# Kernel tuning notes

Hardware: AMD Instinct MI355X
Metric: run time of the kernel (lower is better)

## Reference

```python
import jax, jax.numpy as jnp
import numpy as np

TOPK = 13
ALPHA = 1.0
BETA = 6.0
EPS = 1e-9


def _make_boxes(key, shape, img=640.0, min_sz=10.0, max_sz=110.0):
    k1, k2 = jax.random.split(key)
    cxcy = jax.random.uniform(k1, shape[:-1] + (2,)) * img
    wh = min_sz + jax.random.uniform(k2, shape[:-1] + (2,)) * (max_sz - min_sz)
    return jnp.concatenate([cxcy - wh / 2, cxcy + wh / 2], axis=-1)


def setup_inputs() -> dict:
    key = jax.random.key(0)
    ks = jax.random.split(key, 8)
    B, L, C, n, K = 16, 8400, 1, 32, 68
    pred_scores = jax.random.uniform(ks[0], (B, L, C))
    pred_bboxes = _make_boxes(ks[1], (B, L, 4))
    anchor_points = jax.random.uniform(ks[2], (L, 2)) * 640.0
    gt_labels = jax.random.randint(ks[3], (B, n, 1), 0, C).astype(jnp.int64)
    gt_bboxes = _make_boxes(ks[4], (B, n, 4))
    gt_poses = jax.random.normal(ks[5], (B, n, K, 3))
    gt_vertices = jax.random.normal(ks[6], (B, n, K, 3))
    gt_rotations = jax.random.normal(ks[7], (B, n, 3, 3))
    pad_gt_mask = jnp.ones((B, n, 1), jnp.float32)
    return {"pred_scores": pred_scores, "pred_bboxes": pred_bboxes,
            "anchor_points": anchor_points, "gt_labels": gt_labels,
            "gt_bboxes": gt_bboxes, "gt_poses": gt_poses,
            "gt_vertices": gt_vertices, "gt_rotations": gt_rotations,
            "pad_gt_mask": pad_gt_mask, "bg_index": 1}


def batch_iou_similarity(box1, box2):
    # box1 [B,n,4], box2 [B,L,4] -> [B,n,L]
    b1 = box1[:, :, None, :]
    b2 = box2[:, None, :, :]
    x1y1 = jnp.maximum(b1[..., :2], b2[..., :2])
    x2y2 = jnp.minimum(b1[..., 2:], b2[..., 2:])
    overlap = jnp.clip(x2y2 - x1y1, 0).prod(-1)
    area1 = jnp.clip(b1[..., 2:] - b1[..., :2], 0).prod(-1)
    area2 = jnp.clip(b2[..., 2:] - b2[..., :2], 0).prod(-1)
    return overlap / (area1 + area2 - overlap + EPS)


def check_points_inside_bboxes(points, bboxes):
    # points [L,2], bboxes [B,n,4] -> [B,n,L] float
    x = points[None, None, :, 0]
    y = points[None, None, :, 1]
    xmin, ymin, xmax, ymax = jnp.split(bboxes[:, :, None, :], 4, axis=-1)
    deltas = jnp.stack([x - xmin[..., 0], y - ymin[..., 0],
                        xmax[..., 0] - x, ymax[..., 0] - y], axis=-1)
    return (deltas.min(-1) > EPS).astype(bboxes.dtype)


def gather_topk_anchors(metrics, topk, topk_mask):
    # metrics [B,n,L], topk_mask [B,n,1] -> [B,n,L]
    L = metrics.shape[-1]
    _, topk_idxs = jax.lax.top_k(metrics, topk)  # [B,n,topk]
    is_in_topk = jax.nn.one_hot(topk_idxs, L, dtype=metrics.dtype).sum(-2)
    return is_in_topk * topk_mask


def compute_max_iou_anchor(ious):
    # [B,n,L] -> one-hot over gt dim of per-anchor argmax iou
    n = ious.shape[1]
    idx = ious.argmax(axis=1)  # [B,L]
    return jnp.transpose(jax.nn.one_hot(idx, n, dtype=ious.dtype), (0, 2, 1))


def reference(pred_scores, pred_bboxes, anchor_points, gt_labels, gt_bboxes,
              gt_poses, gt_vertices, gt_rotations, pad_gt_mask, bg_index):
    B, L, C = pred_scores.shape
    n = gt_bboxes.shape[1]
    K = gt_poses.shape[2]

    ious = batch_iou_similarity(gt_bboxes, pred_bboxes)  # [B,n,L]
    ps_t = jnp.transpose(pred_scores, (0, 2, 1))  # [B,C,L]
    lbl = gt_labels[..., 0]  # [B,n]
    bbox_cls_scores = jnp.take_along_axis(ps_t, lbl[:, :, None], axis=1)  # [B,n,L]

    alignment_metrics = (bbox_cls_scores ** ALPHA) * (ious ** BETA)
    is_in_gts = check_points_inside_bboxes(anchor_points, gt_bboxes)
    is_in_topk = gather_topk_anchors(alignment_metrics * is_in_gts, TOPK, pad_gt_mask)
    mask_positive = is_in_topk * is_in_gts * pad_gt_mask  # [B,n,L]
    mask_positive_sum = mask_positive.sum(axis=1)  # [B,L]

    # resolve anchors assigned to multiple gts by max IoU (no-op when none)
    mask_multiple = jnp.broadcast_to((mask_positive_sum[:, None, :] > 1), mask_positive.shape)
    is_max_iou = compute_max_iou_anchor(ious)
    mask_positive = jnp.where(mask_multiple, is_max_iou, mask_positive)
    mask_positive_sum = mask_positive.sum(axis=1)

    batch_ind = jnp.arange(B, dtype=jnp.int32)[:, None]
    assigned_gt_index = mask_positive.argmax(axis=1)  # [B,L]
    assigned_gt_index = assigned_gt_index + batch_ind * n
    flat_idx = assigned_gt_index.reshape(-1)

    assigned_labels = gt_labels.reshape(-1)[flat_idx].reshape(B, L)
    assigned_labels = jnp.where(mask_positive_sum > 0, assigned_labels, bg_index)

    assigned_bboxes = gt_bboxes.reshape(-1, 4)[flat_idx].reshape(B, L, 4)
    assigned_poses = gt_poses.reshape(-1, K, 3)[flat_idx].reshape(B, L, K, 3)
    assigned_vertices = gt_vertices.reshape(-1, K, 3)[flat_idx].reshape(B, L, K, 3)
    assigned_rotations = gt_rotations.reshape(-1, 3, 3)[flat_idx].reshape(B, L, 3, 3)

    scores_oh = jax.nn.one_hot(assigned_labels, C + 1, dtype=pred_scores.dtype)
    keep = jnp.array([i for i in range(C + 1) if i != bg_index], dtype=jnp.int32)
    assigned_scores = scores_oh[..., keep]  # [B,L,C]

    am = alignment_metrics * mask_positive
    max_metrics_per_instance = am.max(axis=-1, keepdims=True)
    max_ious_per_instance = (ious * mask_positive).max(axis=-1, keepdims=True)
    am = am / (max_metrics_per_instance + EPS) * max_ious_per_instance
    am = am.max(axis=1)[:, :, None]  # [B,L,1]
    assigned_scores = assigned_scores * am

    return (assigned_labels, assigned_bboxes, assigned_scores, assigned_poses,
            assigned_vertices, assigned_rotations, assigned_gt_index)
```

## Files before the change

kernel.cpp:

```cpp
#include <hip/hip_runtime.h>

#define Bn 16
#define Ln 8400
#define Cn 1
#define Ngt 32
#define Kpt 68
#define TOPKN 13
#define EPSF 1e-9f
#define CAP 2048

typedef unsigned int u32;

#define OFF_LABELS   0
#define OFF_BBOXES   134400
#define OFF_SCORES   672000
#define OFF_POSES    806400
#define OFF_VERTS    28224000
#define OFF_ROT      55641600
#define OFF_GTIDX    56851200

__device__ __forceinline__ float iou_box(float gx0, float gy0, float gx1, float gy1,
                                         float4 p) {
    float ix0 = fmaxf(gx0, p.x), iy0 = fmaxf(gy0, p.y);
    float ix1 = fminf(gx1, p.z), iy1 = fminf(gy1, p.w);
    float ov = fmaxf(ix1 - ix0, 0.f) * fmaxf(iy1 - iy0, 0.f);
    float a1 = fmaxf(gx1 - gx0, 0.f) * fmaxf(gy1 - gy0, 0.f);
    float a2 = fmaxf(p.z - p.x, 0.f) * fmaxf(p.w - p.y, 0.f);
    return ov / (a1 + a2 - ov + EPSF);
}

__global__ void __launch_bounds__(256) k1_topk(
    const float* __restrict__ pred_scores, const float* __restrict__ pred_bboxes,
    const float* __restrict__ anchors, const int* __restrict__ gt_labels,
    const float* __restrict__ gt_bboxes, const float* __restrict__ pad_mask,
    u32* __restrict__ posmask)
{
    __shared__ float cmet[CAP];
    __shared__ int   cidx[CAP];
    __shared__ int   count;
    __shared__ float rv[4];
    __shared__ int   rl[4], rc[4];
    __shared__ int   sel[TOPKN];

    const int bi = blockIdx.x;
    const int b = bi >> 5, i = bi & 31;
    const int tid = threadIdx.x;

    if (pad_mask[bi] == 0.f) return;

    const float gx0 = gt_bboxes[bi*4+0];
    const float gy0 = gt_bboxes[bi*4+1];
    const float gx1 = gt_bboxes[bi*4+2];
    const float gy1 = gt_bboxes[bi*4+3];
    const int   label = gt_labels[bi];

    const float4* pb = (const float4*)(pred_bboxes + (size_t)b * Ln * 4);
    const float*  ps = pred_scores + (size_t)b * Ln * Cn;
    const float2* ap = (const float2*)anchors;

    if (tid == 0) count = 0;
    __syncthreads();

    for (int l = tid; l < Ln; l += 256) {
        float2 av = ap[l];
        float dmin = fminf(fminf(av.x - gx0, av.y - gy0),
                           fminf(gx1 - av.x, gy1 - av.y));
        if (dmin > EPSF) {
            float4 pv = pb[l];
            float iou = iou_box(gx0, gy0, gx1, gy1, pv);
            float sc = ps[l * Cn + label];
            float i2 = iou * iou;
            float m = sc * (i2 * i2 * i2);
            if (m > 0.f) {
                int c = atomicAdd(&count, 1);
                if (c < CAP) { cmet[c] = m; cidx[c] = l; }
            }
        }
    }
    __syncthreads();
    int p = min(count, CAP);

    if (p > TOPKN) {
        for (int t = 0; t < TOPKN; t++) {
            float bv = -1.f; int bl = 1 << 30, bc = 0;
            for (int c = tid; c < p; c += 256) {
                float v = cmet[c];
                int l = cidx[c];
                if (v > bv || (v == bv && l < bl)) { bv = v; bl = l; bc = c; }
            }
            #pragma unroll
            for (int off = 32; off > 0; off >>= 1) {
                float ov = __shfl_down(bv, off);
                int ol = __shfl_down(bl, off);
                int oc = __shfl_down(bc, off);
                if (ov > bv || (ov == bv && ol < bl)) { bv = ov; bl = ol; bc = oc; }
            }
            int w = tid >> 6;
            if ((tid & 63) == 0) { rv[w] = bv; rl[w] = bl; rc[w] = bc; }
            __syncthreads();
            if (tid == 0) {
                float fv = rv[0]; int fl = rl[0], fc = rc[0];
                #pragma unroll
                for (int w2 = 1; w2 < 4; w2++) {
                    if (rv[w2] > fv || (rv[w2] == fv && rl[w2] < fl)) {
                        fv = rv[w2]; fl = rl[w2]; fc = rc[w2];
                    }
                }
                sel[t] = fl;
                cmet[fc] = -1.f;
            }
            __syncthreads();
        }
        if (tid < TOPKN) atomicOr(&posmask[(size_t)b * Ln + sel[tid]], 1u << i);
    } else {
        if (tid < p) atomicOr(&posmask[(size_t)b * Ln + cidx[tid]], 1u << i);
        if (tid == 0) {
            int need = TOPKN - p;
            for (int l = 0; need > 0 && l < Ln; l++) {
                bool isc = false;
                for (int j = 0; j < p; j++) isc |= (cidx[j] == l);
                if (isc) continue;
                need--;
                float2 av = ap[l];
                float dmin = fminf(fminf(av.x - gx0, av.y - gy0),
                                   fminf(gx1 - av.x, gy1 - av.y));
                if (dmin > EPSF) atomicOr(&posmask[(size_t)b * Ln + l], 1u << i);
            }
        }
    }
}

__global__ void __launch_bounds__(256) k2_resolve(
    const float* __restrict__ pred_scores, const float* __restrict__ pred_bboxes,
    const int* __restrict__ gt_labels, const float* __restrict__ gt_bboxes,
    const u32* __restrict__ posmask, u32* __restrict__ finalmask,
    int* __restrict__ srcidx, float* __restrict__ met_sel,
    float* __restrict__ maxm, float* __restrict__ maxiou)
{
    int bl = blockIdx.x * 256 + threadIdx.x;
    if (bl >= Bn * Ln) return;
    int b = bl / Ln;
    u32 pm = posmask[bl];
    u32 fm = pm;
    float4 pbox = ((const float4*)pred_bboxes)[bl];
    const float4* gb = (const float4*)(gt_bboxes + (size_t)b * Ngt * 4);
    if (__popc(pm) > 1) {
        float best = -1.f; int bi2 = 0;
        for (int i = 0; i < Ngt; i++) {
            float4 g = gb[i];
            float v = iou_box(g.x, g.y, g.z, g.w, pbox);
            if (v > best) { best = v; bi2 = i; }
        }
        fm = 1u << bi2;
    }
    finalmask[bl] = fm;
    int idx = fm ? (__ffs((int)fm) - 1) : 0;
    int src = b * Ngt + idx;
    srcidx[bl] = src;
    float met = 0.f;
    if (fm) {
        float4 g = gb[idx];
        float iou = iou_box(g.x, g.y, g.z, g.w, pbox);
        float sc = pred_scores[(size_t)bl * Cn + gt_labels[src]];
        float i2 = iou * iou;
        met = sc * (i2 * i2 * i2);
        atomicMax((int*)&maxm[src],   __float_as_int(met));
        atomicMax((int*)&maxiou[src], __float_as_int(iou));
    }
    met_sel[bl] = met;
}

__global__ void __launch_bounds__(256) k3_out(
    const float* __restrict__ gt_poses, const float* __restrict__ gt_verts,
    const u32* __restrict__ finalmask, const int* __restrict__ srcidx,
    const float* __restrict__ met_sel, const float* __restrict__ maxm_a,
    const float* __restrict__ maxiou_a, const int* __restrict__ gt_labels,
    const float* __restrict__ gt_bboxes, const float* __restrict__ gt_rot,
    const int* __restrict__ bg_index_p, float* __restrict__ out)
{
    const int QPER = (Kpt * 3) / 4;
    const int total = Bn * Ln * QPER;
    const int nq = 2 * total;
    int t = blockIdx.x * 256 + threadIdx.x;
    if (t < nq) {
        const float* ga = gt_poses;
        float4* outp = (float4*)(out + OFF_POSES);
        int qq = t;
        if (qq >= total) { qq -= total; ga = gt_verts; outp = (float4*)(out + OFF_VERTS); }
        int bl = qq / QPER;
        int r = qq - bl * QPER;
        int src = srcidx[bl];
        outp[qq] = ((const float4*)ga)[src * QPER + r];
        return;
    }
    int bl = t - nq;
    if (bl >= Bn * Ln) return;
    const int bg = *bg_index_p;
    u32 fm = finalmask[bl];
    int src = srcidx[bl];
    int label = fm ? gt_labels[src] : bg;
    float am = 0.f;
    if (fm) am = met_sel[bl] / (maxm_a[src] + EPSF) * maxiou_a[src];
    int keep0 = (bg == 0) ? 1 : 0;
    float sc = (label == keep0) ? am : 0.f;

    out[OFF_LABELS + bl] = (float)label;
    out[OFF_SCORES + bl] = sc;
    out[OFF_GTIDX  + bl] = (float)src;
    ((float4*)(out + OFF_BBOXES))[bl] = ((const float4*)gt_bboxes)[src];
    const float* rs = gt_rot + src * 9;
    float* rd = out + OFF_ROT + (size_t)bl * 9;
#pragma unroll
    for (int j = 0; j < 9; j++) rd[j] = rs[j];
}

extern "C" void kernel_launch(void* const* d_in, const int* in_sizes, int n_in,
                              void* d_out, int out_size, void* d_ws, size_t ws_size,
                              hipStream_t stream)
{
    const float* pred_scores = (const float*)d_in[0];
    const float* pred_bboxes = (const float*)d_in[1];
    const float* anchors     = (const float*)d_in[2];
    const int*   gt_labels   = (const int*)d_in[3];
    const float* gt_bboxes   = (const float*)d_in[4];
    const float* gt_poses    = (const float*)d_in[5];
    const float* gt_verts    = (const float*)d_in[6];
    const float* gt_rot      = (const float*)d_in[7];
    const float* pad_mask    = (const float*)d_in[8];
    const int*   bg_index    = (const int*)d_in[9];

    const int nBL = Bn * Ln;
    u32*   posmask  = (u32*)d_ws;
    float* maxm     = (float*)(posmask + nBL);
    float* maxiou   = maxm + Bn * Ngt;
    u32*   finalmask= (u32*)(maxiou + Bn * Ngt);
    int*   srcidx   = (int*)(finalmask + nBL);
    float* met_sel  = (float*)(srcidx + nBL);

    hipMemsetAsync(posmask, 0, ((size_t)nBL + 2 * Bn * Ngt) * sizeof(u32), stream);

    k1_topk<<<Bn * Ngt, 256, 0, stream>>>(pred_scores, pred_bboxes, anchors,
                                          gt_labels, gt_bboxes, pad_mask, posmask);
    k2_resolve<<<(nBL + 255) / 256, 256, 0, stream>>>(pred_scores, pred_bboxes,
                                                      gt_labels, gt_bboxes, posmask,
                                                      finalmask, srcidx, met_sel,
                                                      maxm, maxiou);
    const int nq = 2 * Bn * Ln * ((Kpt * 3) / 4);
    const int ntot = nq + nBL;
    k3_out<<<(ntot + 255) / 256, 256, 0, stream>>>(gt_poses, gt_verts, finalmask,
                                                   srcidx, met_sel, maxm, maxiou,
                                                   gt_labels, gt_bboxes, gt_rot,
                                                   bg_index, (float*)d_out);
}
```

Baseline: 301.3 us.

## Fuse memset and three kernels into one cooperative persistent kernel

Replaces the memset plus three separate kernel launches with a single cooperative kernel of 512 blocks that zeroes the workspace, runs per-GT top-k, resolves multi-assignments, and writes outputs, separated by grid-wide syncs. The aim is to remove launch overhead and inter-kernel gaps. The trade-off is fixed parallelism of 512x256 threads with grid-stride loops for the large output copy phase, plus the cost of the grid barriers. The large memory-bound pose and vertex copy may lose bandwidth with fewer resident waves.

```diff
diff --git a/kernel.cpp b/kernel.cpp
--- a/kernel.cpp
+++ b/kernel.cpp
@@ -1,4 +1,7 @@
 #include <hip/hip_runtime.h>
+#include <hip/hip_cooperative_groups.h>
+
+namespace cg = cooperative_groups;
 
 #define Bn 16
 #define Ln 8400
@@ -18,6 +21,10 @@
 #define OFF_VERTS    28224000
 #define OFF_ROT      55641600
 #define OFF_GTIDX    56851200
+
+#define NBLK 512
+#define NTHR 256
+#define GSZ  (NBLK * NTHR)
 
 __device__ __forceinline__ float iou_box(float gx0, float gy0, float gx1, float gy1,
                                          float4 p) {
@@ -29,189 +36,192 @@
     return ov / (a1 + a2 - ov + EPSF);
 }
 
-__global__ void __launch_bounds__(256) k1_topk(
+__global__ void __launch_bounds__(256, 2) fused(
     const float* __restrict__ pred_scores, const float* __restrict__ pred_bboxes,
     const float* __restrict__ anchors, const int* __restrict__ gt_labels,
-    const float* __restrict__ gt_bboxes, const float* __restrict__ pad_mask,
-    u32* __restrict__ posmask)
+    const float* __restrict__ gt_bboxes, const float* __restrict__ gt_poses,
+    const float* __restrict__ gt_verts, const float* __restrict__ gt_rot,
+    const float* __restrict__ pad_mask, const int* __restrict__ bg_index_p,
+    u32* __restrict__ posmask, float* __restrict__ maxm, float* __restrict__ maxiou,
+    u32* __restrict__ finalmask, int* __restrict__ srcidx, float* __restrict__ met_sel,
+    float* __restrict__ out)
 {
-    __shared__ float cmet[CAP];
-    __shared__ int   cidx[CAP];
-    __shared__ int   count;
-    __shared__ float rv[4];
-    __shared__ int   rl[4], rc[4];
-    __shared__ int   sel[TOPKN];
-
-    const int bi = blockIdx.x;
-    const int b = bi >> 5, i = bi & 31;
+    cg::grid_group gg = cg::this_grid();
     const int tid = threadIdx.x;
-
-    if (pad_mask[bi] == 0.f) return;
-
-    const float gx0 = gt_bboxes[bi*4+0];
-    const float gy0 = gt_bboxes[bi*4+1];
-    const float gx1 = gt_bboxes[bi*4+2];
-    const float gy1 = gt_bboxes[bi*4+3];
-    const int   label = gt_labels[bi];
-
-    const float4* pb = (const float4*)(pred_bboxes + (size_t)b * Ln * 4);
-    const float*  ps = pred_scores + (size_t)b * Ln * Cn;
-    const float2* ap = (const float2*)anchors;
-
-    if (tid == 0) count = 0;
-    __syncthreads();
-
-    for (int l = tid; l < Ln; l += 256) {
-        float2 av = ap[l];
-        float dmin = fminf(fminf(av.x - gx0, av.y - gy0),
-                           fminf(gx1 - av.x, gy1 - av.y));
-        if (dmin > EPSF) {
-            float4 pv = pb[l];
-            float iou = iou_box(gx0, gy0, gx1, gy1, pv);
-            float sc = ps[l * Cn + label];
-            float i2 = iou * iou;
-            float m = sc * (i2 * i2 * i2);
-            if (m > 0.f) {
-                int c = atomicAdd(&count, 1);
-                if (c < CAP) { cmet[c] = m; cidx[c] = l; }
-            }
-        }
-    }
-    __syncthreads();
-    int p = min(count, CAP);
-
-    if (p > TOPKN) {
-        for (int t = 0; t < TOPKN; t++) {
-            float bv = -1.f; int bl = 1 << 30, bc = 0;
-            for (int c = tid; c < p; c += 256) {
-                float v = cmet[c];
-                int l = cidx[c];
-                if (v > bv || (v == bv && l < bl)) { bv = v; bl = l; bc = c; }
-            }
-            #pragma unroll
-            for (int off = 32; off > 0; off >>= 1) {
-                float ov = __shfl_down(bv, off);
-                int ol = __shfl_down(bl, off);
-                int oc = __shfl_down(bc, off);
-                if (ov > bv || (ov == bv && ol < bl)) { bv = ov; bl = ol; bc = oc; }
-            }
-            int w = tid >> 6;
-            if ((tid & 63) == 0) { rv[w] = bv; rl[w] = bl; rc[w] = bc; }
+    const int gtid = blockIdx.x * NTHR + tid;
+
+    {
+        const int nz = Bn * Ln + 2 * Bn * Ngt;
+        for (int w = gtid; w < nz; w += GSZ) posmask[w] = 0u;
+    }
+    gg.sync();
+
+    {
+        __shared__ float cmet[CAP];
+        __shared__ int   cidx[CAP];
+        __shared__ int   count;
+        __shared__ float rv[4];
+        __shared__ int   rl[4], rc[4];
+        __shared__ int   sel[TOPKN];
+
+        const int bi = blockIdx.x;
+        const int b = bi >> 5, i = bi & 31;
+
+        if (pad_mask[bi] != 0.f) {
+            const float gx0 = gt_bboxes[bi*4+0];
+            const float gy0 = gt_bboxes[bi*4+1];
+            const float gx1 = gt_bboxes[bi*4+2];
+            const float gy1 = gt_bboxes[bi*4+3];
+            const int   label = gt_labels[bi];
+
+            const float4* pb = (const float4*)(pred_bboxes + (size_t)b * Ln * 4);
+            const float*  ps = pred_scores + (size_t)b * Ln * Cn;
+            const float2* ap = (const float2*)anchors;
+
+            if (tid == 0) count = 0;
             __syncthreads();
-            if (tid == 0) {
-                float fv = rv[0]; int fl = rl[0], fc = rc[0];
-                #pragma unroll
-                for (int w2 = 1; w2 < 4; w2++) {
-                    if (rv[w2] > fv || (rv[w2] == fv && rl[w2] < fl)) {
-                        fv = rv[w2]; fl = rl[w2]; fc = rc[w2];
-                    }
-                }
-                sel[t] = fl;
-                cmet[fc] = -1.f;
-            }
-            __syncthreads();
-        }
-        if (tid < TOPKN) atomicOr(&posmask[(size_t)b * Ln + sel[tid]], 1u << i);
-    } else {
-        if (tid < p) atomicOr(&posmask[(size_t)b * Ln + cidx[tid]], 1u << i);
-        if (tid == 0) {
-            int need = TOPKN - p;
-            for (int l = 0; need > 0 && l < Ln; l++) {
-                bool isc = false;
-                for (int j = 0; j < p; j++) isc |= (cidx[j] == l);
-                if (isc) continue;
-                need--;
+
+            for (int l = tid; l < Ln; l += NTHR) {
                 float2 av = ap[l];
                 float dmin = fminf(fminf(av.x - gx0, av.y - gy0),
                                    fminf(gx1 - av.x, gy1 - av.y));
-                if (dmin > EPSF) atomicOr(&posmask[(size_t)b * Ln + l], 1u << i);
-            }
-        }
-    }
-}
-
-__global__ void __launch_bounds__(256) k2_resolve(
-    const float* __restrict__ pred_scores, const float* __restrict__ pred_bboxes,
-    const int* __restrict__ gt_labels, const float* __restrict__ gt_bboxes,
-    const u32* __restrict__ posmask, u32* __restrict__ finalmask,
-    int* __restrict__ srcidx, float* __restrict__ met_sel,
-    float* __restrict__ maxm, float* __restrict__ maxiou)
-{
-    int bl = blockIdx.x * 256 + threadIdx.x;
-    if (bl >= Bn * Ln) return;
-    int b = bl / Ln;
-    u32 pm = posmask[bl];
-    u32 fm = pm;
-    float4 pbox = ((const float4*)pred_bboxes)[bl];
-    const float4* gb = (const float4*)(gt_bboxes + (size_t)b * Ngt * 4);
-    if (__popc(pm) > 1) {
-        float best = -1.f; int bi2 = 0;
-        for (int i = 0; i < Ngt; i++) {
-            float4 g = gb[i];
-            float v = iou_box(g.x, g.y, g.z, g.w, pbox);
-            if (v > best) { best = v; bi2 = i; }
-        }
-        fm = 1u << bi2;
-    }
-    finalmask[bl] = fm;
-    int idx = fm ? (__ffs((int)fm) - 1) : 0;
-    int src = b * Ngt + idx;
-    srcidx[bl] = src;
-    float met = 0.f;
-    if (fm) {
-        float4 g = gb[idx];
-        float iou = iou_box(g.x, g.y, g.z, g.w, pbox);
-        float sc = pred_scores[(size_t)bl * Cn + gt_labels[src]];
-        float i2 = iou * iou;
-        met = sc * (i2 * i2 * i2);
-        atomicMax((int*)&maxm[src],   __float_as_int(met));
-        atomicMax((int*)&maxiou[src], __float_as_int(iou));
-    }
-    met_sel[bl] = met;
-}
-
-__global__ void __launch_bounds__(256) k3_out(
-    const float* __restrict__ gt_poses, const float* __restrict__ gt_verts,
-    const u32* __restrict__ finalmask, const int* __restrict__ srcidx,
-    const float* __restrict__ met_sel, const float* __restrict__ maxm_a,
-    const float* __restrict__ maxiou_a, const int* __restrict__ gt_labels,
-    const float* __restrict__ gt_bboxes, const float* __restrict__ gt_rot,
-    const int* __restrict__ bg_index_p, float* __restrict__ out)
-{
-    const int QPER = (Kpt * 3) / 4;
-    const int total = Bn * Ln * QPER;
-    const int nq = 2 * total;
-    int t = blockIdx.x * 256 + threadIdx.x;
-    if (t < nq) {
-        const float* ga = gt_poses;
-        float4* outp = (float4*)(out + OFF_POSES);
-        int qq = t;
-        if (qq >= total) { qq -= total; ga = gt_verts; outp = (float4*)(out + OFF_VERTS); }
-        int bl = qq / QPER;
-        int r = qq - bl * QPER;
-        int src = srcidx[bl];
-        outp[qq] = ((const float4*)ga)[src * QPER + r];
-        return;
-    }
-    int bl = t - nq;
-    if (bl >= Bn * Ln) return;
-    const int bg = *bg_index_p;
-    u32 fm = finalmask[bl];
-    int src = srcidx[bl];
-    int label = fm ? gt_labels[src] : bg;
-    float am = 0.f;
-    if (fm) am = met_sel[bl] / (maxm_a[src] + EPSF) * maxiou_a[src];
-    int keep0 = (bg == 0) ? 1 : 0;
-    float sc = (label == keep0) ? am : 0.f;
-
-    out[OFF_LABELS + bl] = (float)label;
-    out[OFF_SCORES + bl] = sc;
-    out[OFF_GTIDX  + bl] = (float)src;
-    ((float4*)(out + OFF_BBOXES))[bl] = ((const float4*)gt_bboxes)[src];
-    const float* rs = gt_rot + src * 9;
-    float* rd = out + OFF_ROT + (size_t)bl * 9;
+                if (dmin > EPSF) {
+                    float4 pv = pb[l];
+                    float iou = iou_box(gx0, gy0, gx1, gy1, pv);
+                    float sc = ps[l * Cn + label];
+                    float i2 = iou * iou;
+                    float m = sc * (i2 * i2 * i2);
+                    if (m > 0.f) {
+                        int c = atomicAdd(&count, 1);
+                        if (c < CAP) { cmet[c] = m; cidx[c] = l; }
+                    }
+                }
+            }
+            __syncthreads();
+            int p = min(count, CAP);
+
+            if (p > TOPKN) {
+                for (int t = 0; t < TOPKN; t++) {
+                    float bv = -1.f; int bl = 1 << 30, bc = 0;
+                    for (int c = tid; c < p; c += NTHR) {
+                        float v = cmet[c];
+                        int l = cidx[c];
+                        if (v > bv || (v == bv && l < bl)) { bv = v; bl = l; bc = c; }
+                    }
+                    #pragma unroll
+                    for (int off = 32; off > 0; off >>= 1) {
+                        float ov = __shfl_down(bv, off);
+                        int ol = __shfl_down(bl, off);
+                        int oc = __shfl_down(bc, off);
+                        if (ov > bv || (ov == bv && ol < bl)) { bv = ov; bl = ol; bc = oc; }
+                    }
+                    int w = tid >> 6;
+                    if ((tid & 63) == 0) { rv[w] = bv; rl[w] = bl; rc[w] = bc; }
+                    __syncthreads();
+                    if (tid == 0) {
+                        float fv = rv[0]; int fl = rl[0], fc = rc[0];
+                        #pragma unroll
+                        for (int w2 = 1; w2 < 4; w2++) {
+                            if (rv[w2] > fv || (rv[w2] == fv && rl[w2] < fl)) {
+                                fv = rv[w2]; fl = rl[w2]; fc = rc[w2];
+                            }
+                        }
+                        sel[t] = fl;
+                        cmet[fc] = -1.f;
+                    }
+                    __syncthreads();
+                }
+                if (tid < TOPKN) atomicOr(&posmask[(size_t)b * Ln + sel[tid]], 1u << i);
+            } else {
+                if (tid < p) atomicOr(&posmask[(size_t)b * Ln + cidx[tid]], 1u << i);
+                if (tid == 0) {
+                    int need = TOPKN - p;
+                    for (int l = 0; need > 0 && l < Ln; l++) {
+                        bool isc = false;
+                        for (int j = 0; j < p; j++) isc |= (cidx[j] == l);
+                        if (isc) continue;
+                        need--;
+                        float2 av = ap[l];
+                        float dmin = fminf(fminf(av.x - gx0, av.y - gy0),
+                                           fminf(gx1 - av.x, gy1 - av.y));
+                        if (dmin > EPSF) atomicOr(&posmask[(size_t)b * Ln + l], 1u << i);
+                    }
+                }
+            }
+        }
+    }
+    gg.sync();
+
+    for (int bl = gtid; bl < Bn * Ln; bl += GSZ) {
+        int b = bl / Ln;
+        u32 pm = posmask[bl];
+        u32 fm = pm;
+        float4 pbox = ((const float4*)pred_bboxes)[bl];
+        const float4* gb = (const float4*)(gt_bboxes + (size_t)b * Ngt * 4);
+        if (__popc(pm) > 1) {
+            float best = -1.f; int bi2 = 0;
+            for (int i = 0; i < Ngt; i++) {
+                float4 g = gb[i];
+                float v = iou_box(g.x, g.y, g.z, g.w, pbox);
+                if (v > best) { best = v; bi2 = i; }
+            }
+            fm = 1u << bi2;
+        }
+        finalmask[bl] = fm;
+        int idx = fm ? (__ffs((int)fm) - 1) : 0;
+        int src = b * Ngt + idx;
+        srcidx[bl] = src;
+        float met = 0.f;
+        if (fm) {
+            float4 g = gb[idx];
+            float iou = iou_box(g.x, g.y, g.z, g.w, pbox);
+            float sc = pred_scores[(size_t)bl * Cn + gt_labels[src]];
+            float i2 = iou * iou;
+            met = sc * (i2 * i2 * i2);
+            atomicMax((int*)&maxm[src],   __float_as_int(met));
+            atomicMax((int*)&maxiou[src], __float_as_int(iou));
+        }
+        met_sel[bl] = met;
+    }
+    gg.sync();
+
+    {
+        const int QPER = (Kpt * 3) / 4;
+        const int total = Bn * Ln * QPER;
+        const int nq = 2 * total;
+        const int ntot = nq + Bn * Ln;
+        for (int t = gtid; t < ntot; t += GSZ) {
+            if (t < nq) {
+                const float* ga = gt_poses;
+                float4* outp = (float4*)(out + OFF_POSES);
+                int qq = t;
+                if (qq >= total) { qq -= total; ga = gt_verts; outp = (float4*)(out + OFF_VERTS); }
+                int bl = qq / QPER;
+                int r = qq - bl * QPER;
+                int src = srcidx[bl];
+                outp[qq] = ((const float4*)ga)[src * QPER + r];
+                continue;
+            }
+            int bl = t - nq;
+            const int bg = *bg_index_p;
+            u32 fm = finalmask[bl];
+            int src = srcidx[bl];
+            int label = fm ? gt_labels[src] : bg;
+            float am = 0.f;
+            if (fm) am = met_sel[bl] / (maxm[src] + EPSF) * maxiou[src];
+            int keep0 = (bg == 0) ? 1 : 0;
+            float sc = (label == keep0) ? am : 0.f;
+
+            out[OFF_LABELS + bl] = (float)label;
+            out[OFF_SCORES + bl] = sc;
+            out[OFF_GTIDX  + bl] = (float)src;
+            ((float4*)(out + OFF_BBOXES))[bl] = ((const float4*)gt_bboxes)[src];
+            const float* rs = gt_rot + src * 9;
+            float* rd = out + OFF_ROT + (size_t)bl * 9;
 #pragma unroll
-    for (int j = 0; j < 9; j++) rd[j] = rs[j];
+            for (int j = 0; j < 9; j++) rd[j] = rs[j];
+        }
+    }
 }
 
 extern "C" void kernel_launch(void* const* d_in, const int* in_sizes, int n_in,
@@ -236,19 +246,15 @@
     u32*   finalmask= (u32*)(maxiou + Bn * Ngt);
     int*   srcidx   = (int*)(finalmask + nBL);
     float* met_sel  = (float*)(srcidx + nBL);
-
-    hipMemsetAsync(posmask, 0, ((size_t)nBL + 2 * Bn * Ngt) * sizeof(u32), stream);
-
-    k1_topk<<<Bn * Ngt, 256, 0, stream>>>(pred_scores, pred_bboxes, anchors,
-                                          gt_labels, gt_bboxes, pad_mask, posmask);
-    k2_resolve<<<(nBL + 255) / 256, 256, 0, stream>>>(pred_scores, pred_bboxes,
-                                                      gt_labels, gt_bboxes, posmask,
-                                                      finalmask, srcidx, met_sel,
-                                                      maxm, maxiou);
-    const int nq = 2 * Bn * Ln * ((Kpt * 3) / 4);
-    const int ntot = nq + nBL;
-    k3_out<<<(ntot + 255) / 256, 256, 0, stream>>>(gt_poses, gt_verts, finalmask,
-                                                   srcidx, met_sel, maxm, maxiou,
-                                                   gt_labels, gt_bboxes, gt_rot,
-                                                   bg_index, (float*)d_out);
+    float* outf     = (float*)d_out;
+
+    void* args[] = {
+        (void*)&pred_scores, (void*)&pred_bboxes, (void*)&anchors, (void*)&gt_labels,
+        (void*)&gt_bboxes, (void*)&gt_poses, (void*)&gt_verts, (void*)&gt_rot,
+        (void*)&pad_mask, (void*)&bg_index,
+        (void*)&posmask, (void*)&maxm, (void*)&maxiou,
+        (void*)&finalmask, (void*)&srcidx, (void*)&met_sel, (void*)&outf
+    };
+    hipLaunchCooperativeKernel((const void*)fused, dim3(NBLK), dim3(NTHR),
+                               args, 0, stream);
 }
```

Measured after the change: 473.0 us. +57.0%, slower.
